# Optimization experiments

Hardware: AMD Instinct MI355X
Metric: run time of the kernel (lower is better)

The kernel has to match this reference:

```python
import jax, jax.numpy as jnp
import numpy as np

NEG_SLOPE = 0.2  # PyG GATConv default negative_slope


def _gat_layer(x, src, dst, W, a_src, a_dst, b, num_nodes):
    # x: [N, Fin] -> h: [N, Fout]
    h = x @ W
    # per-node attention logits (heads=1)
    alpha_s = h @ a_src  # [N]
    alpha_d = h @ a_dst  # [N]
    # edge scores e_ij = LeakyReLU(a_src . h_j + a_dst . h_i), j=src, i=dst
    e = alpha_s[src] + alpha_d[dst]
    e = jnp.where(e >= 0, e, NEG_SLOPE * e)
    # segment softmax over edges sharing the same destination node
    e_max = jax.ops.segment_max(e, dst, num_segments=num_nodes)  # [N]
    w = jnp.exp(e - e_max[dst])  # [E]
    denom = jax.ops.segment_sum(w, dst, num_segments=num_nodes)  # [N]
    alpha = w / denom[dst]  # [E]
    # weighted scatter-sum of source messages into destinations
    out = jax.ops.segment_sum(h[src] * alpha[:, None], dst, num_segments=num_nodes)
    return out + b


def _add_self_loops(edge_index, num_nodes):
    loops = jnp.arange(num_nodes, dtype=edge_index.dtype)
    src = jnp.concatenate([edge_index[0], loops])
    dst = jnp.concatenate([edge_index[1], loops])
    return src, dst


def setup_inputs() -> dict:
    key = jax.random.key(0)
    ks = jax.random.split(key, 8)
    N, E, F_in, F_hid, F_out = 50000, 800000, 128, 128, 64
    inp = {
        "node_features": jax.random.normal(ks[0], (N, F_in), dtype=jnp.float32),
        "edge_index": jax.random.randint(ks[1], (2, E), 0, N, dtype=jnp.int32),
        "W1": jax.random.normal(ks[2], (F_in, F_hid), dtype=jnp.float32) / np.sqrt(F_in),
        "a_src1": jax.random.normal(ks[3], (F_hid,), dtype=jnp.float32) / np.sqrt(F_hid),
        "a_dst1": jax.random.normal(ks[4], (F_hid,), dtype=jnp.float32) / np.sqrt(F_hid),
        "b1": jnp.zeros((F_hid,), dtype=jnp.float32),
        "W2": jax.random.normal(ks[5], (F_hid, F_out), dtype=jnp.float32) / np.sqrt(F_hid),
        "a_src2": jax.random.normal(ks[6], (F_out,), dtype=jnp.float32) / np.sqrt(F_out),
        "a_dst2": jax.random.normal(ks[7], (F_out,), dtype=jnp.float32) / np.sqrt(F_out),
        "b2": jnp.zeros((F_out,), dtype=jnp.float32),
    }
    return inp


def reference(node_features, edge_index, W1, a_src1, a_dst1, b1, W2, a_src2, a_dst2, b2):
    num_nodes = node_features.shape[0]
    src, dst = _add_self_loops(edge_index, num_nodes)
    x = _gat_layer(node_features, src, dst, W1, a_src1, a_dst1, b1, num_nodes)
    x = jax.nn.relu(x)
    x = _gat_layer(x, src, dst, W2, a_src2, a_dst2, b2, num_nodes)
    return x
```

## Files before the change

kernel.cpp:

```cpp
#include <hip/hip_runtime.h>
#include <hip/hip_fp16.h>
#include <cstddef>

#define NEG_SLOPE 0.2f
#define TILE 4096
#define CSR_CAP 6144

typedef _Float16 h8 __attribute__((ext_vector_type(8)));
typedef _Float16 h4 __attribute__((ext_vector_type(4)));
typedef float f4 __attribute__((ext_vector_type(4)));

__device__ __forceinline__ float leaky(float x) { return x >= 0.f ? x : NEG_SLOPE * x; }

__device__ __forceinline__ int wave_iscan(int v, int lane) {
#pragma unroll
    for (int off = 1; off < 64; off <<= 1) {
        int t = __shfl_up(v, off);
        if (lane >= off) v += t;
    }
    return v;
}

__global__ __launch_bounds__(256) void prep(
    const float* __restrict__ W1, const float* __restrict__ W2,
    _Float16* __restrict__ W1t, _Float16* __restrict__ W2t,
    int* __restrict__ bfill)
{
    const int b = blockIdx.x;
    const int tid = threadIdx.x;
    if (b == 0) bfill[tid] = 0;
    if (b < 8) {
        for (int i = b * 2048 + tid; i < (b + 1) * 2048; i += 256) {
            int n = i >> 7, k = i & 127;
            W1t[n * 128 + k] = (_Float16)W1[k * 128 + n];
        }
    } else {
        const int bb = b - 8;
        for (int i = bb * 2048 + tid; i < (bb + 1) * 2048; i += 256) {
            int n = i >> 7, k = i & 127;
            W2t[n * 128 + k] = (_Float16)W2[k * 64 + n];
        }
    }
}

__global__ __launch_bounds__(256) void gemm1_scatter(
    const float* __restrict__ x, const _Float16* __restrict__ Wg,
    const float* __restrict__ a_s, const float* __restrict__ a_d,
    _Float16* __restrict__ hh, float* __restrict__ alphaS, float* __restrict__ alphaD,
    int N, int nblk_gemm,
    const int* __restrict__ src, const int* __restrict__ dst,
    int* __restrict__ bfill, unsigned* __restrict__ staging, int cap, int E)
{
    constexpr int K = 128;
    constexpr int LDK = K + 8;
    constexpr int F = 128;
    constexpr int NT = F / 16;

    __shared__ union {
        struct { _Float16 As[64 * LDK]; _Float16 Wt[F * LDK]; } g;
        struct {
            int lcnt[256]; int loff[256]; int gbase[256]; int ws[4];
            unsigned pairs[TILE]; unsigned char bkt[TILE];
        } s;
    } u;

    const int tid = threadIdx.x;

    if (blockIdx.x < (unsigned)nblk_gemm) {
        const int wave = tid >> 6;
        const int lane = tid & 63;
        const int q = lane >> 4;
        const int c = lane & 15;
        const int rowb = blockIdx.x * 64;

        for (int i = tid; i < 64 * (K / 4); i += 256) {
            int r = i >> 5, c4 = i & 31;
            int gr = rowb + r;
            float4 v = (gr < N) ? *(const float4*)(x + (size_t)gr * K + c4 * 4)
                                : make_float4(0.f, 0.f, 0.f, 0.f);
            h4 hv = { (_Float16)v.x, (_Float16)v.y, (_Float16)v.z, (_Float16)v.w };
            *(h4*)(u.g.As + r * LDK + c4 * 4) = hv;
        }
        for (int i = tid; i < F * (K / 8); i += 256) {
            int n = i >> 4, k8 = i & 15;
            *(h8*)(u.g.Wt + n * LDK + k8 * 8) = *(const h8*)(Wg + n * 128 + k8 * 8);
        }
        __syncthreads();

        f4 acc[NT];
#pragma unroll
        for (int nt = 0; nt < NT; nt++) acc[nt] = (f4)0.f;

        const _Float16* aw = u.g.As + (wave * 16 + c) * LDK + q * 8;
#pragma unroll
        for (int kt = 0; kt < 4; kt++) {
            h8 af = *(const h8*)(aw + kt * 32);
#pragma unroll
            for (int nt = 0; nt < NT; nt++) {
                h8 bf = *(const h8*)(u.g.Wt + (nt * 16 + c) * LDK + kt * 32 + q * 8);
                acc[nt] = __builtin_amdgcn_mfma_f32_16x16x32_f16(af, bf, acc[nt], 0, 0, 0);
            }
        }

        float asl[NT], adl[NT];
#pragma unroll
        for (int nt = 0; nt < NT; nt++) {
            asl[nt] = a_s[nt * 16 + c];
            adl[nt] = a_d[nt * 16 + c];
        }
        const int row0 = rowb + wave * 16 + q * 4;
#pragma unroll
        for (int r = 0; r < 4; r++) {
            int row = row0 + r;
            if (row < N) {
                float ps = 0.f, pd = 0.f;
#pragma unroll
                for (int nt = 0; nt < NT; nt++) {
                    float v = acc[nt][r];
                    hh[(size_t)row * F + nt * 16 + c] = (_Float16)v;
                    ps += v * asl[nt];
                    pd += v * adl[nt];
                }
#pragma unroll
                for (int off = 8; off >= 1; off >>= 1) {
                    ps += __shfl_down(ps, off, 16);
                    pd += __shfl_down(pd, off, 16);
                }
                if (c == 0) { alphaS[row] = ps; alphaD[row] = pd; }
            }
        }
    } else {
        const int base = (blockIdx.x - nblk_gemm) * TILE;
        const int vt = min(TILE, E - base);

        u.s.lcnt[tid] = 0;
        __syncthreads();

        int d[TILE / 256], s[TILE / 256], r[TILE / 256];
#pragma unroll
        for (int j = 0; j < TILE / 256; j++) {
            int idx = base + j * 256 + tid;
            if (idx < E) {
                d[j] = dst[idx]; s[j] = src[idx];
                r[j] = atomicAdd(&u.s.lcnt[d[j] >> 8], 1);
            } else d[j] = -1;
        }
        __syncthreads();
        {
            int lane = tid & 63, wid = tid >> 6;
            int v = u.s.lcnt[tid];
            int incl = wave_iscan(v, lane);
            if (lane == 63) u.s.ws[wid] = incl;
            __syncthreads();
            int woff = 0;
            for (int w = 0; w < wid; w++) woff += u.s.ws[w];
            u.s.loff[tid] = woff + incl - v;
        }
        __syncthreads();
        {
            int c = u.s.lcnt[tid];
            if (c > 0) u.s.gbase[tid] = tid * cap + atomicAdd(&bfill[tid], c);
        }
        __syncthreads();
#pragma unroll
        for (int j = 0; j < TILE / 256; j++) {
            if (d[j] >= 0) {
                int b = d[j] >> 8;
                int slot = u.s.loff[b] + r[j];
                u.s.pairs[slot] = ((unsigned)d[j] << 16) | (unsigned)s[j];
                u.s.bkt[slot] = (unsigned char)b;
            }
        }
        __syncthreads();
        for (int slot = tid; slot < vt; slot += 256) {
            int b = u.s.bkt[slot];
            staging[u.s.gbase[b] + (slot - u.s.loff[b])] = u.s.pairs[slot];
        }
    }
}

template <int F, typename IT>
__global__ __launch_bounds__(256) void gemm_mfma(
    const IT* __restrict__ x, const _Float16* __restrict__ Wg,
    const float* __restrict__ a_s, const float* __restrict__ a_d,
    _Float16* __restrict__ hh, float* __restrict__ alphaS, float* __restrict__ alphaD,
    int N)
{
    constexpr int K = 128;
    constexpr int LDK = K + 8;
    constexpr int NT = F / 16;

    __shared__ _Float16 As[64 * LDK];
    __shared__ _Float16 Wt[F * LDK];

    const int tid = threadIdx.x;
    const int wave = tid >> 6;
    const int lane = tid & 63;
    const int q = lane >> 4;
    const int c = lane & 15;
    const int rowb = blockIdx.x * 64;

    if constexpr (sizeof(IT) == 4) {
        for (int i = tid; i < 64 * (K / 4); i += 256) {
            int r = i >> 5, c4 = i & 31;
            int gr = rowb + r;
            float4 v = (gr < N) ? *(const float4*)((const float*)x + (size_t)gr * K + c4 * 4)
                                : make_float4(0.f, 0.f, 0.f, 0.f);
            h4 hv = { (_Float16)v.x, (_Float16)v.y, (_Float16)v.z, (_Float16)v.w };
            *(h4*)(As + r * LDK + c4 * 4) = hv;
        }
    } else {
        for (int i = tid; i < 64 * (K / 8); i += 256) {
            int r = i >> 4, c8 = i & 15;
            int gr = rowb + r;
            h8 v;
            if (gr < N) v = *(const h8*)((const _Float16*)x + (size_t)gr * K + c8 * 8);
            else        v = (h8)(_Float16)0.f;
            *(h8*)(As + r * LDK + c8 * 8) = v;
        }
    }
    for (int i = tid; i < F * (K / 8); i += 256) {
        int n = i >> 4, k8 = i & 15;
        *(h8*)(Wt + n * LDK + k8 * 8) = *(const h8*)(Wg + n * 128 + k8 * 8);
    }
    __syncthreads();

    f4 acc[NT];
#pragma unroll
    for (int nt = 0; nt < NT; nt++) acc[nt] = (f4)0.f;

    const _Float16* aw = As + (wave * 16 + c) * LDK + q * 8;
#pragma unroll
    for (int kt = 0; kt < 4; kt++) {
        h8 af = *(const h8*)(aw + kt * 32);
#pragma unroll
        for (int nt = 0; nt < NT; nt++) {
            h8 bf = *(const h8*)(Wt + (nt * 16 + c) * LDK + kt * 32 + q * 8);
            acc[nt] = __builtin_amdgcn_mfma_f32_16x16x32_f16(af, bf, acc[nt], 0, 0, 0);
        }
    }

    float asl[NT], adl[NT];
#pragma unroll
    for (int nt = 0; nt < NT; nt++) {
        asl[nt] = a_s[nt * 16 + c];
        adl[nt] = a_d[nt * 16 + c];
    }
    const int row0 = rowb + wave * 16 + q * 4;
#pragma unroll
    for (int r = 0; r < 4; r++) {
        int row = row0 + r;
        if (row < N) {
            float ps = 0.f, pd = 0.f;
#pragma unroll
            for (int nt = 0; nt < NT; nt++) {
                float v = acc[nt][r];
                hh[(size_t)row * F + nt * 16 + c] = (_Float16)v;
                ps += v * asl[nt];
                pd += v * adl[nt];
            }
#pragma unroll
            for (int off = 8; off >= 1; off >>= 1) {
                ps += __shfl_down(ps, off, 16);
                pd += __shfl_down(pd, off, 16);
            }
            if (c == 0) { alphaS[row] = ps; alphaD[row] = pd; }
        }
    }
}

__global__ __launch_bounds__(512) void bucket_to_csr(
    const unsigned* __restrict__ staging, const int* __restrict__ bfill,
    int* __restrict__ row_start, int* __restrict__ row_end,
    int* __restrict__ src_sorted, int cap, int N)
{
    __shared__ unsigned lp[CSR_CAP];
    __shared__ int lcnt[256], loff[256], lfill[256];
    __shared__ int ws[4];
    const int tid = threadIdx.x;
    const int b = blockIdx.x;
    const int beg = b * cap;
    const int len = bfill[b];

    if (tid < 256) lcnt[tid] = 0;
    __syncthreads();
    for (int p = tid; p < len; p += 512) {
        unsigned u = staging[beg + p];
        lp[p] = u;
        atomicAdd(&lcnt[(u >> 16) & 255], 1);
    }
    __syncthreads();
    {
        int lane = tid & 63, wid = tid >> 6;
        int v = 0, incl = 0;
        if (tid < 256) {
            v = lcnt[tid];
            incl = wave_iscan(v, lane);
            if (lane == 63) ws[wid] = incl;
        }
        __syncthreads();
        if (tid < 256) {
            int woff = 0;
            for (int w = 0; w < wid; w++) woff += ws[w];
            int excl = woff + incl - v;
            loff[tid] = excl;
            lfill[tid] = excl;
            int node = (b << 8) + tid;
            if (node < N) { row_start[node] = beg + excl; row_end[node] = beg + excl + v; }
        }
    }
    __syncthreads();
    for (int p = tid; p < len; p += 512) {
        unsigned u = lp[p];
        int pos = atomicAdd(&lfill[(u >> 16) & 255], 1);
        src_sorted[beg + pos] = (int)(u & 0xFFFFu);
    }
}

template <int F, bool RELU, typename OT>
__global__ __launch_bounds__(256) void gat_aggregate(
    const int* __restrict__ row_start, const int* __restrict__ row_end,
    const int* __restrict__ src_sorted, const __half* __restrict__ hh,
    const float* __restrict__ aS, const float* __restrict__ aD,
    const float* __restrict__ bias, OT* __restrict__ out, int N)
{
    constexpr int LPE = F / 8;
    constexpr int EPW = 64 / LPE;

    const int i = blockIdx.x * 4 + (threadIdx.x >> 6);
    if (i >= N) return;
    const int lane = threadIdx.x & 63;
    const int sub = lane / LPE;
    const int l = lane % LPE;

    const float adi = aD[i];
    const int start = row_start[i];
    const int end = row_end[i];

    float accA[8], accB[8];
#pragma unroll
    for (int q = 0; q < 8; q++) { accA[q] = 0.f; accB[q] = 0.f; }
    float denA = 0.f, denB = 0.f;

    int e = start + sub;
    int s0 = (e + 0 * EPW < end) ? src_sorted[e + 0 * EPW] : -1;
    int s1 = (e + 1 * EPW < end) ? src_sorted[e + 1 * EPW] : -1;
    int s2 = (e + 2 * EPW < end) ? src_sorted[e + 2 * EPW] : -1;
    int s3 = (e + 3 * EPW < end) ? src_sorted[e + 3 * EPW] : -1;

    while (s0 >= 0) {
        int eb = e + 4 * EPW;
        int n0 = (eb + 0 * EPW < end) ? src_sorted[eb + 0 * EPW] : -1;
        int n1 = (eb + 1 * EPW < end) ? src_sorted[eb + 1 * EPW] : -1;
        int n2 = (eb + 2 * EPW < end) ? src_sorted[eb + 2 * EPW] : -1;
        int n3 = (eb + 3 * EPW < end) ? src_sorted[eb + 3 * EPW] : -1;

        {
            float w = __expf(leaky(aS[s0] + adi));
            uint4 u = *(const uint4*)(hh + (size_t)s0 * F + l * 8);
            const __half2* hp = (const __half2*)&u;
#pragma unroll
            for (int q = 0; q < 4; q++) {
                float2 f = __half22float2(hp[q]);
                accA[q * 2] += w * f.x; accA[q * 2 + 1] += w * f.y;
            }
            denA += w;
        }
        if (s1 >= 0) {
            float w = __expf(leaky(aS[s1] + adi));
            uint4 u = *(const uint4*)(hh + (size_t)s1 * F + l * 8);
            const __half2* hp = (const __half2*)&u;
#pragma unroll
            for (int q = 0; q < 4; q++) {
                float2 f = __half22float2(hp[q]);
                accB[q * 2] += w * f.x; accB[q * 2 + 1] += w * f.y;
            }
            denB += w;
        }
        if (s2 >= 0) {
            float w = __expf(leaky(aS[s2] + adi));
            uint4 u = *(const uint4*)(hh + (size_t)s2 * F + l * 8);
            const __half2* hp = (const __half2*)&u;
#pragma unroll
            for (int q = 0; q < 4; q++) {
                float2 f = __half22float2(hp[q]);
                accA[q * 2] += w * f.x; accA[q * 2 + 1] += w * f.y;
            }
            denA += w;
        }
        if (s3 >= 0) {
            float w = __expf(leaky(aS[s3] + adi));
            uint4 u = *(const uint4*)(hh + (size_t)s3 * F + l * 8);
            const __half2* hp = (const __half2*)&u;
#pragma unroll
            for (int q = 0; q < 4; q++) {
                float2 f = __half22float2(hp[q]);
                accB[q * 2] += w * f.x; accB[q * 2 + 1] += w * f.y;
            }
            denB += w;
        }
        e = eb;
        s0 = n0; s1 = n1; s2 = n2; s3 = n3;
    }

    float acc[8];
#pragma unroll
    for (int q = 0; q < 8; q++) acc[q] = accA[q] + accB[q];
    float denom = denA + denB;

#pragma unroll
    for (int off = 32; off >= LPE; off >>= 1) {
#pragma unroll
        for (int q = 0; q < 8; q++) acc[q] += __shfl_down(acc[q], off);
        denom += __shfl_down(denom, off);
    }

    if (sub == 0) {
        float wsf = __expf(leaky(aS[i] + adi));
        uint4 u = *(const uint4*)(hh + (size_t)i * F + l * 8);
        const __half2* hp = (const __half2*)&u;
        float inv = 1.f / (denom + wsf);
        float4 b0 = *(const float4*)(bias + l * 8);
        float4 b1 = *(const float4*)(bias + l * 8 + 4);
        float o[8];
#pragma unroll
        for (int q = 0; q < 4; q++) {
            float2 f = __half22float2(hp[q]);
            o[q * 2]     = (acc[q * 2]     + wsf * f.x) * inv;
            o[q * 2 + 1] = (acc[q * 2 + 1] + wsf * f.y) * inv;
        }
        o[0] += b0.x; o[1] += b0.y; o[2] += b0.z; o[3] += b0.w;
        o[4] += b1.x; o[5] += b1.y; o[6] += b1.z; o[7] += b1.w;
        if (RELU) {
#pragma unroll
            for (int q = 0; q < 8; q++) o[q] = fmaxf(o[q], 0.f);
        }
        if constexpr (sizeof(OT) == 2) {
            __half2 qh[4];
            qh[0] = __floats2half2_rn(o[0], o[1]);
            qh[1] = __floats2half2_rn(o[2], o[3]);
            qh[2] = __floats2half2_rn(o[4], o[5]);
            qh[3] = __floats2half2_rn(o[6], o[7]);
            *(uint4*)((__half*)out + (size_t)i * F + l * 8) = *(uint4*)qh;
        } else {
            *(float4*)((float*)out + (size_t)i * F + l * 8)     = make_float4(o[0], o[1], o[2], o[3]);
            *(float4*)((float*)out + (size_t)i * F + l * 8 + 4) = make_float4(o[4], o[5], o[6], o[7]);
        }
    }
}

extern "C" void kernel_launch(void* const* d_in, const int* in_sizes, int n_in,
                              void* d_out, int out_size, void* d_ws, size_t ws_size,
                              hipStream_t stream)
{
    const float* x   = (const float*)d_in[0];
    const int*   ei  = (const int*)d_in[1];
    const float* W1  = (const float*)d_in[2];
    const float* aS1 = (const float*)d_in[3];
    const float* aD1 = (const float*)d_in[4];
    const float* b1  = (const float*)d_in[5];
    const float* W2  = (const float*)d_in[6];
    const float* aS2 = (const float*)d_in[7];
    const float* aD2 = (const float*)d_in[8];
    const float* b2  = (const float*)d_in[9];

    const int K = 128, F1 = 128, F2 = 64;
    const int N = in_sizes[0] / K;
    const int E = in_sizes[1] / 2;
    const int* src = ei;
    const int* dst = ei + E;

    const int Np = (N + 4) & ~3;
    const int NB = (N + 255) >> 8;
    const int nbt = (E + TILE - 1) / TILE;
    const int nblk_gemm = (N + 63) / 64;
    int cap = (((E / NB) * 3) / 2 + 255) & ~255;
    if (cap > CSR_CAP) cap = CSR_CAP;

    char* wsb = (char*)d_ws;
    int* bfill        = (int*)wsb;      wsb += 256 * 4;
    _Float16* W1t     = (_Float16*)wsb; wsb += 128 * 128 * 2;
    _Float16* W2t     = (_Float16*)wsb; wsb += 64 * 128 * 2;
    int* row_start    = (int*)wsb;      wsb += (size_t)Np * 4;
    int* row_end      = (int*)wsb;      wsb += (size_t)Np * 4;
    unsigned* staging = (unsigned*)wsb; wsb += (size_t)NB * CSR_CAP * 4;
    int* src_sorted   = (int*)wsb;      wsb += (size_t)NB * CSR_CAP * 4;
    _Float16* hh1     = (_Float16*)wsb; wsb += (size_t)N * F1 * 2;
    _Float16* x2h     = (_Float16*)wsb; wsb += (size_t)N * F1 * 2;
    _Float16* hh2     = (_Float16*)wsb; wsb += (size_t)N * F2 * 2;
    float* as_        = (float*)wsb;    wsb += (size_t)Np * 4;
    float* ad_        = (float*)wsb;    wsb += (size_t)Np * 4;

    dim3 blk(256);

    prep<<<dim3(12), blk, 0, stream>>>(W1, W2, W1t, W2t, bfill);

    gemm1_scatter<<<dim3(nblk_gemm + nbt), blk, 0, stream>>>(
        x, W1t, aS1, aD1, hh1, as_, ad_, N, nblk_gemm,
        src, dst, bfill, staging, cap, E);

    bucket_to_csr<<<dim3(NB), dim3(512), 0, stream>>>(staging, bfill, row_start, row_end,
                                                      src_sorted, cap, N);

    gat_aggregate<F1, true, __half><<<dim3((N + 3) / 4), blk, 0, stream>>>(
        row_start, row_end, src_sorted, (const __half*)hh1, as_, ad_, b1,
        (__half*)x2h, N);

    gemm_mfma<F2, _Float16><<<dim3((N + 63) / 64), blk, 0, stream>>>(
        x2h, W2t, aS2, aD2, hh2, as_, ad_, N);

    gat_aggregate<F2, false, float><<<dim3((N + 3) / 4), blk, 0, stream>>>(
        row_start, row_end, src_sorted, (const __half*)hh2, as_, ad_, b2,
        (float*)d_out, N);
}
```

Measured before the change: 190.9 us.

## Fuse layer-1 aggregation with layer-2 GEMM and widen CSR build blocks

Measured after the change: 202.0 us. 5.8% more time.

```diff
diff --git a/kernel.cpp b/kernel.cpp
--- a/kernel.cpp
+++ b/kernel.cpp
@@ -179,97 +179,7 @@
     }
 }
 
-template <int F, typename IT>
-__global__ __launch_bounds__(256) void gemm_mfma(
-    const IT* __restrict__ x, const _Float16* __restrict__ Wg,
-    const float* __restrict__ a_s, const float* __restrict__ a_d,
-    _Float16* __restrict__ hh, float* __restrict__ alphaS, float* __restrict__ alphaD,
-    int N)
-{
-    constexpr int K = 128;
-    constexpr int LDK = K + 8;
-    constexpr int NT = F / 16;
-
-    __shared__ _Float16 As[64 * LDK];
-    __shared__ _Float16 Wt[F * LDK];
-
-    const int tid = threadIdx.x;
-    const int wave = tid >> 6;
-    const int lane = tid & 63;
-    const int q = lane >> 4;
-    const int c = lane & 15;
-    const int rowb = blockIdx.x * 64;
-
-    if constexpr (sizeof(IT) == 4) {
-        for (int i = tid; i < 64 * (K / 4); i += 256) {
-            int r = i >> 5, c4 = i & 31;
-            int gr = rowb + r;
-            float4 v = (gr < N) ? *(const float4*)((const float*)x + (size_t)gr * K + c4 * 4)
-                                : make_float4(0.f, 0.f, 0.f, 0.f);
-            h4 hv = { (_Float16)v.x, (_Float16)v.y, (_Float16)v.z, (_Float16)v.w };
-            *(h4*)(As + r * LDK + c4 * 4) = hv;
-        }
-    } else {
-        for (int i = tid; i < 64 * (K / 8); i += 256) {
-            int r = i >> 4, c8 = i & 15;
-            int gr = rowb + r;
-            h8 v;
-            if (gr < N) v = *(const h8*)((const _Float16*)x + (size_t)gr * K + c8 * 8);
-            else        v = (h8)(_Float16)0.f;
-            *(h8*)(As + r * LDK + c8 * 8) = v;
-        }
-    }
-    for (int i = tid; i < F * (K / 8); i += 256) {
-        int n = i >> 4, k8 = i & 15;
-        *(h8*)(Wt + n * LDK + k8 * 8) = *(const h8*)(Wg + n * 128 + k8 * 8);
-    }
-    __syncthreads();
-
-    f4 acc[NT];
-#pragma unroll
-    for (int nt = 0; nt < NT; nt++) acc[nt] = (f4)0.f;
-
-    const _Float16* aw = As + (wave * 16 + c) * LDK + q * 8;
-#pragma unroll
-    for (int kt = 0; kt < 4; kt++) {
-        h8 af = *(const h8*)(aw + kt * 32);
-#pragma unroll
-        for (int nt = 0; nt < NT; nt++) {
-            h8 bf = *(const h8*)(Wt + (nt * 16 + c) * LDK + kt * 32 + q * 8);
-            acc[nt] = __builtin_amdgcn_mfma_f32_16x16x32_f16(af, bf, acc[nt], 0, 0, 0);
-        }
-    }
-
-    float asl[NT], adl[NT];
-#pragma unroll
-    for (int nt = 0; nt < NT; nt++) {
-        asl[nt] = a_s[nt * 16 + c];
-        adl[nt] = a_d[nt * 16 + c];
-    }
-    const int row0 = rowb + wave * 16 + q * 4;
-#pragma unroll
-    for (int r = 0; r < 4; r++) {
-        int row = row0 + r;
-        if (row < N) {
-            float ps = 0.f, pd = 0.f;
-#pragma unroll
-            for (int nt = 0; nt < NT; nt++) {
-                float v = acc[nt][r];
-                hh[(size_t)row * F + nt * 16 + c] = (_Float16)v;
-                ps += v * asl[nt];
-                pd += v * adl[nt];
-            }
-#pragma unroll
-            for (int off = 8; off >= 1; off >>= 1) {
-                ps += __shfl_down(ps, off, 16);
-                pd += __shfl_down(pd, off, 16);
-            }
-            if (c == 0) { alphaS[row] = ps; alphaD[row] = pd; }
-        }
-    }
-}
-
-__global__ __launch_bounds__(512) void bucket_to_csr(
+__global__ __launch_bounds__(1024) void bucket_to_csr(
     const unsigned* __restrict__ staging, const int* __restrict__ bfill,
     int* __restrict__ row_start, int* __restrict__ row_end,
     int* __restrict__ src_sorted, int cap, int N)
@@ -284,7 +194,7 @@
 
     if (tid < 256) lcnt[tid] = 0;
     __syncthreads();
-    for (int p = tid; p < len; p += 512) {
+    for (int p = tid; p < len; p += 1024) {
         unsigned u = staging[beg + p];
         lp[p] = u;
         atomicAdd(&lcnt[(u >> 16) & 255], 1);
@@ -310,10 +220,199 @@
         }
     }
     __syncthreads();
-    for (int p = tid; p < len; p += 512) {
+    for (int p = tid; p < len; p += 1024) {
         unsigned u = lp[p];
         int pos = atomicAdd(&lfill[(u >> 16) & 255], 1);
         src_sorted[beg + pos] = (int)(u & 0xFFFFu);
+    }
+}
+
+__global__ __launch_bounds__(256) void agg1_gemm2(
+    const int* __restrict__ row_start, const int* __restrict__ row_end,
+    const int* __restrict__ src_sorted, const __half* __restrict__ hh1,
+    const float* __restrict__ aS1, const float* __restrict__ aD1,
+    const float* __restrict__ b1,
+    const _Float16* __restrict__ W2t,
+    const float* __restrict__ aS2, const float* __restrict__ aD2,
+    _Float16* __restrict__ hh2, float* __restrict__ alphaS2, float* __restrict__ alphaD2,
+    int N)
+{
+    constexpr int K = 128;
+    constexpr int LDK = K + 8;
+    constexpr int F2 = 64;
+    constexpr int NT = F2 / 16;
+
+    __shared__ _Float16 As[64 * LDK];
+    __shared__ _Float16 Wt[F2 * LDK];
+
+    const int tid = threadIdx.x;
+    const int wave = tid >> 6;
+    const int lane = tid & 63;
+    const int rowb = blockIdx.x * 64;
+
+    for (int i = tid; i < F2 * (K / 8); i += 256) {
+        int n = i >> 4, k8 = i & 15;
+        *(h8*)(Wt + n * LDK + k8 * 8) = *(const h8*)(W2t + n * 128 + k8 * 8);
+    }
+
+    const int sub = lane >> 4;
+    const int l = lane & 15;
+
+    for (int it = 0; it < 16; it++) {
+        const int r = wave * 16 + it;
+        const int i = rowb + r;
+        if (i < N) {
+            const float adi = aD1[i];
+            const int start = row_start[i];
+            const int end = row_end[i];
+
+            float accA[8], accB[8];
+#pragma unroll
+            for (int q = 0; q < 8; q++) { accA[q] = 0.f; accB[q] = 0.f; }
+            float denA = 0.f, denB = 0.f;
+
+            int e = start + sub;
+            int s0 = (e + 0 * 4 < end) ? src_sorted[e + 0 * 4] : -1;
+            int s1 = (e + 1 * 4 < end) ? src_sorted[e + 1 * 4] : -1;
+            int s2 = (e + 2 * 4 < end) ? src_sorted[e + 2 * 4] : -1;
+            int s3 = (e + 3 * 4 < end) ? src_sorted[e + 3 * 4] : -1;
+
+            while (s0 >= 0) {
+                int eb = e + 16;
+                int n0 = (eb + 0 * 4 < end) ? src_sorted[eb + 0 * 4] : -1;
+                int n1 = (eb + 1 * 4 < end) ? src_sorted[eb + 1 * 4] : -1;
+                int n2 = (eb + 2 * 4 < end) ? src_sorted[eb + 2 * 4] : -1;
+                int n3 = (eb + 3 * 4 < end) ? src_sorted[eb + 3 * 4] : -1;
+
+                {
+                    float w = __expf(leaky(aS1[s0] + adi));
+                    uint4 u = *(const uint4*)(hh1 + (size_t)s0 * 128 + l * 8);
+                    const __half2* hp = (const __half2*)&u;
+#pragma unroll
+                    for (int q = 0; q < 4; q++) {
+                        float2 f = __half22float2(hp[q]);
+                        accA[q * 2] += w * f.x; accA[q * 2 + 1] += w * f.y;
+                    }
+                    denA += w;
+                }
+                if (s1 >= 0) {
+                    float w = __expf(leaky(aS1[s1] + adi));
+                    uint4 u = *(const uint4*)(hh1 + (size_t)s1 * 128 + l * 8);
+                    const __half2* hp = (const __half2*)&u;
+#pragma unroll
+                    for (int q = 0; q < 4; q++) {
+                        float2 f = __half22float2(hp[q]);
+                        accB[q * 2] += w * f.x; accB[q * 2 + 1] += w * f.y;
+                    }
+                    denB += w;
+                }
+                if (s2 >= 0) {
+                    float w = __expf(leaky(aS1[s2] + adi));
+                    uint4 u = *(const uint4*)(hh1 + (size_t)s2 * 128 + l * 8);
+                    const __half2* hp = (const __half2*)&u;
+#pragma unroll
+                    for (int q = 0; q < 4; q++) {
+                        float2 f = __half22float2(hp[q]);
+                        accA[q * 2] += w * f.x; accA[q * 2 + 1] += w * f.y;
+                    }
+                    denA += w;
+                }
+                if (s3 >= 0) {
+                    float w = __expf(leaky(aS1[s3] + adi));
+                    uint4 u = *(const uint4*)(hh1 + (size_t)s3 * 128 + l * 8);
+                    const __half2* hp = (const __half2*)&u;
+#pragma unroll
+                    for (int q = 0; q < 4; q++) {
+                        float2 f = __half22float2(hp[q]);
+                        accB[q * 2] += w * f.x; accB[q * 2 + 1] += w * f.y;
+                    }
+                    denB += w;
+                }
+                e = eb;
+                s0 = n0; s1 = n1; s2 = n2; s3 = n3;
+            }
+
+            float acc[8];
+#pragma unroll
+            for (int q = 0; q < 8; q++) acc[q] = accA[q] + accB[q];
+            float denom = denA + denB;
+
+#pragma unroll
+            for (int off = 32; off >= 16; off >>= 1) {
+#pragma unroll
+                for (int q = 0; q < 8; q++) acc[q] += __shfl_down(acc[q], off);
+                denom += __shfl_down(denom, off);
+            }
+
+            if (sub == 0) {
+                float wsf = __expf(leaky(aS1[i] + adi));
+                uint4 u = *(const uint4*)(hh1 + (size_t)i * 128 + l * 8);
+                const __half2* hp = (const __half2*)&u;
+                float inv = 1.f / (denom + wsf);
+                float4 b0 = *(const float4*)(b1 + l * 8);
+                float4 bb1 = *(const float4*)(b1 + l * 8 + 4);
+                float o[8];
+#pragma unroll
+                for (int q = 0; q < 4; q++) {
+                    float2 f = __half22float2(hp[q]);
+                    o[q * 2]     = (acc[q * 2]     + wsf * f.x) * inv;
+                    o[q * 2 + 1] = (acc[q * 2 + 1] + wsf * f.y) * inv;
+                }
+                o[0] += b0.x; o[1] += b0.y; o[2] += b0.z; o[3] += b0.w;
+                o[4] += bb1.x; o[5] += bb1.y; o[6] += bb1.z; o[7] += bb1.w;
+                h8 hv;
+#pragma unroll
+                for (int q = 0; q < 8; q++) hv[q] = (_Float16)fmaxf(o[q], 0.f);
+                *(h8*)(As + r * LDK + l * 8) = hv;
+            }
+        }
+    }
+    __syncthreads();
+
+    const int q = lane >> 4;
+    const int c = lane & 15;
+
+    f4 acc[NT];
+#pragma unroll
+    for (int nt = 0; nt < NT; nt++) acc[nt] = (f4)0.f;
+
+    const _Float16* aw = As + (wave * 16 + c) * LDK + q * 8;
+#pragma unroll
+    for (int kt = 0; kt < 4; kt++) {
+        h8 af = *(const h8*)(aw + kt * 32);
+#pragma unroll
+        for (int nt = 0; nt < NT; nt++) {
+            h8 bf = *(const h8*)(Wt + (nt * 16 + c) * LDK + kt * 32 + q * 8);
+            acc[nt] = __builtin_amdgcn_mfma_f32_16x16x32_f16(af, bf, acc[nt], 0, 0, 0);
+        }
+    }
+
+    float asl[NT], adl[NT];
+#pragma unroll
+    for (int nt = 0; nt < NT; nt++) {
+        asl[nt] = aS2[nt * 16 + c];
+        adl[nt] = aD2[nt * 16 + c];
+    }
+    const int row0 = rowb + wave * 16 + q * 4;
+#pragma unroll
+    for (int r = 0; r < 4; r++) {
+        int row = row0 + r;
+        if (row < N) {
+            float ps = 0.f, pd = 0.f;
+#pragma unroll
+            for (int nt = 0; nt < NT; nt++) {
+                float v = acc[nt][r];
+                hh2[(size_t)row * F2 + nt * 16 + c] = (_Float16)v;
+                ps += v * asl[nt];
+                pd += v * adl[nt];
+            }
+#pragma unroll
+            for (int off = 8; off >= 1; off >>= 1) {
+                ps += __shfl_down(ps, off, 16);
+                pd += __shfl_down(pd, off, 16);
+            }
+            if (c == 0) { alphaS2[row] = ps; alphaD2[row] = pd; }
+        }
     }
 }
 
@@ -486,10 +585,11 @@
     unsigned* staging = (unsigned*)wsb; wsb += (size_t)NB * CSR_CAP * 4;
     int* src_sorted   = (int*)wsb;      wsb += (size_t)NB * CSR_CAP * 4;
     _Float16* hh1     = (_Float16*)wsb; wsb += (size_t)N * F1 * 2;
-    _Float16* x2h     = (_Float16*)wsb; wsb += (size_t)N * F1 * 2;
     _Float16* hh2     = (_Float16*)wsb; wsb += (size_t)N * F2 * 2;
     float* as_        = (float*)wsb;    wsb += (size_t)Np * 4;
     float* ad_        = (float*)wsb;    wsb += (size_t)Np * 4;
+    float* as2_       = (float*)wsb;    wsb += (size_t)Np * 4;
+    float* ad2_       = (float*)wsb;    wsb += (size_t)Np * 4;
 
     dim3 blk(256);
 
@@ -499,17 +599,14 @@
         x, W1t, aS1, aD1, hh1, as_, ad_, N, nblk_gemm,
         src, dst, bfill, staging, cap, E);
 
-    bucket_to_csr<<<dim3(NB), dim3(512), 0, stream>>>(staging, bfill, row_start, row_end,
-                                                      src_sorted, cap, N);
-
-    gat_aggregate<F1, true, __half><<<dim3((N + 3) / 4), blk, 0, stream>>>(
+    bucket_to_csr<<<dim3(NB), dim3(1024), 0, stream>>>(staging, bfill, row_start, row_end,
+                                                       src_sorted, cap, N);
+
+    agg1_gemm2<<<dim3(nblk_gemm), blk, 0, stream>>>(
         row_start, row_end, src_sorted, (const __half*)hh1, as_, ad_, b1,
-        (__half*)x2h, N);
-
-    gemm_mfma<F2, _Float16><<<dim3((N + 63) / 64), blk, 0, stream>>>(
-        x2h, W2t, aS2, aD2, hh2, as_, ad_, N);
+        W2t, aS2, aD2, hh2, as2_, ad2_, N);
 
     gat_aggregate<F2, false, float><<<dim3((N + 3) / 4), blk, 0, stream>>>(
-        row_start, row_end, src_sorted, (const __half*)hh2, as_, ad_, b2,
+        row_start, row_end, src_sorted, (const __half*)hh2, as2_, ad2_, b2,
         (float*)d_out, N);
 }
```

## Split layer-1 GEMM across scatter and CSR kernels to balance load

Applied to the files above, without the earlier changes.

Measured after the change: 189.2 us. Within noise of the previous version (-0.9%).

```diff
diff --git a/kernel.cpp b/kernel.cpp
--- a/kernel.cpp
+++ b/kernel.cpp
@@ -43,21 +43,93 @@
     }
 }
 
-__global__ __launch_bounds__(256) void gemm1_scatter(
+struct GemmLds { _Float16 As[64 * 136]; _Float16 Wt[128 * 136]; };
+
+__device__ __forceinline__ void gemm1_tile(
+    GemmLds& g, int tid, int rowb,
     const float* __restrict__ x, const _Float16* __restrict__ Wg,
     const float* __restrict__ a_s, const float* __restrict__ a_d,
     _Float16* __restrict__ hh, float* __restrict__ alphaS, float* __restrict__ alphaD,
-    int N, int nblk_gemm,
-    const int* __restrict__ src, const int* __restrict__ dst,
-    int* __restrict__ bfill, unsigned* __restrict__ staging, int cap, int E)
+    int N)
 {
     constexpr int K = 128;
     constexpr int LDK = K + 8;
     constexpr int F = 128;
     constexpr int NT = F / 16;
 
+    const int wave = tid >> 6;
+    const int lane = tid & 63;
+    const int q = lane >> 4;
+    const int c = lane & 15;
+
+    for (int i = tid; i < 64 * (K / 4); i += 256) {
+        int r = i >> 5, c4 = i & 31;
+        int gr = rowb + r;
+        float4 v = (gr < N) ? *(const float4*)(x + (size_t)gr * K + c4 * 4)
+                            : make_float4(0.f, 0.f, 0.f, 0.f);
+        h4 hv = { (_Float16)v.x, (_Float16)v.y, (_Float16)v.z, (_Float16)v.w };
+        *(h4*)(g.As + r * LDK + c4 * 4) = hv;
+    }
+    for (int i = tid; i < F * (K / 8); i += 256) {
+        int n = i >> 4, k8 = i & 15;
+        *(h8*)(g.Wt + n * LDK + k8 * 8) = *(const h8*)(Wg + n * 128 + k8 * 8);
+    }
+    __syncthreads();
+
+    f4 acc[NT];
+#pragma unroll
+    for (int nt = 0; nt < NT; nt++) acc[nt] = (f4)0.f;
+
+    const _Float16* aw = g.As + (wave * 16 + c) * LDK + q * 8;
+#pragma unroll
+    for (int kt = 0; kt < 4; kt++) {
+        h8 af = *(const h8*)(aw + kt * 32);
+#pragma unroll
+        for (int nt = 0; nt < NT; nt++) {
+            h8 bf = *(const h8*)(g.Wt + (nt * 16 + c) * LDK + kt * 32 + q * 8);
+            acc[nt] = __builtin_amdgcn_mfma_f32_16x16x32_f16(af, bf, acc[nt], 0, 0, 0);
+        }
+    }
+
+    float asl[NT], adl[NT];
+#pragma unroll
+    for (int nt = 0; nt < NT; nt++) {
+        asl[nt] = a_s[nt * 16 + c];
+        adl[nt] = a_d[nt * 16 + c];
+    }
+    const int row0 = rowb + wave * 16 + q * 4;
+#pragma unroll
+    for (int r = 0; r < 4; r++) {
+        int row = row0 + r;
+        if (row < N) {
+            float ps = 0.f, pd = 0.f;
+#pragma unroll
+            for (int nt = 0; nt < NT; nt++) {
+                float v = acc[nt][r];
+                hh[(size_t)row * F + nt * 16 + c] = (_Float16)v;
+                ps += v * asl[nt];
+                pd += v * adl[nt];
+            }
+#pragma unroll
+            for (int off = 8; off >= 1; off >>= 1) {
+                ps += __shfl_down(ps, off, 16);
+                pd += __shfl_down(pd, off, 16);
+            }
+            if (c == 0) { alphaS[row] = ps; alphaD[row] = pd; }
+        }
+    }
+}
+
+__global__ __launch_bounds__(256) void fatA(
+    const float* __restrict__ x, const _Float16* __restrict__ Wg,
+    const float* __restrict__ a_s, const float* __restrict__ a_d,
+    _Float16* __restrict__ hh, float* __restrict__ alphaS, float* __restrict__ alphaD,
+    int N, int gsplit,
+    const int* __restrict__ src, const int* __restrict__ dst,
+    int* __restrict__ bfill, unsigned* __restrict__ staging, int cap, int E)
+{
     __shared__ union {
-        struct { _Float16 As[64 * LDK]; _Float16 Wt[F * LDK]; } g;
+        GemmLds g;
         struct {
             int lcnt[256]; int loff[256]; int gbase[256]; int ws[4];
             unsigned pairs[TILE]; unsigned char bkt[TILE];
@@ -66,71 +138,10 @@
 
     const int tid = threadIdx.x;
 
-    if (blockIdx.x < (unsigned)nblk_gemm) {
-        const int wave = tid >> 6;
-        const int lane = tid & 63;
-        const int q = lane >> 4;
-        const int c = lane & 15;
-        const int rowb = blockIdx.x * 64;
-
-        for (int i = tid; i < 64 * (K / 4); i += 256) {
-            int r = i >> 5, c4 = i & 31;
-            int gr = rowb + r;
-            float4 v = (gr < N) ? *(const float4*)(x + (size_t)gr * K + c4 * 4)
-                                : make_float4(0.f, 0.f, 0.f, 0.f);
-            h4 hv = { (_Float16)v.x, (_Float16)v.y, (_Float16)v.z, (_Float16)v.w };
-            *(h4*)(u.g.As + r * LDK + c4 * 4) = hv;
-        }
-        for (int i = tid; i < F * (K / 8); i += 256) {
-            int n = i >> 4, k8 = i & 15;
-            *(h8*)(u.g.Wt + n * LDK + k8 * 8) = *(const h8*)(Wg + n * 128 + k8 * 8);
-        }
-        __syncthreads();
-
-        f4 acc[NT];
-#pragma unroll
-        for (int nt = 0; nt < NT; nt++) acc[nt] = (f4)0.f;
-
-        const _Float16* aw = u.g.As + (wave * 16 + c) * LDK + q * 8;
-#pragma unroll
-        for (int kt = 0; kt < 4; kt++) {
-            h8 af = *(const h8*)(aw + kt * 32);
-#pragma unroll
-            for (int nt = 0; nt < NT; nt++) {
-                h8 bf = *(const h8*)(u.g.Wt + (nt * 16 + c) * LDK + kt * 32 + q * 8);
-                acc[nt] = __builtin_amdgcn_mfma_f32_16x16x32_f16(af, bf, acc[nt], 0, 0, 0);
-            }
-        }
-
-        float asl[NT], adl[NT];
-#pragma unroll
-        for (int nt = 0; nt < NT; nt++) {
-            asl[nt] = a_s[nt * 16 + c];
-            adl[nt] = a_d[nt * 16 + c];
-        }
-        const int row0 = rowb + wave * 16 + q * 4;
-#pragma unroll
-        for (int r = 0; r < 4; r++) {
-            int row = row0 + r;
-            if (row < N) {
-                float ps = 0.f, pd = 0.f;
-#pragma unroll
-                for (int nt = 0; nt < NT; nt++) {
-                    float v = acc[nt][r];
-                    hh[(size_t)row * F + nt * 16 + c] = (_Float16)v;
-                    ps += v * asl[nt];
-                    pd += v * adl[nt];
-                }
-#pragma unroll
-                for (int off = 8; off >= 1; off >>= 1) {
-                    ps += __shfl_down(ps, off, 16);
-                    pd += __shfl_down(pd, off, 16);
-                }
-                if (c == 0) { alphaS[row] = ps; alphaD[row] = pd; }
-            }
-        }
+    if (blockIdx.x < (unsigned)gsplit) {
+        gemm1_tile(u.g, tid, blockIdx.x * 64, x, Wg, a_s, a_d, hh, alphaS, alphaD, N);
     } else {
-        const int base = (blockIdx.x - nblk_gemm) * TILE;
+        const int base = (blockIdx.x - gsplit) * TILE;
         const int vt = min(TILE, E - base);
 
         u.s.lcnt[tid] = 0;
@@ -179,6 +190,64 @@
     }
 }
 
+__global__ __launch_bounds__(256) void fatB(
+    const float* __restrict__ x, const _Float16* __restrict__ Wg,
+    const float* __restrict__ a_s, const float* __restrict__ a_d,
+    _Float16* __restrict__ hh, float* __restrict__ alphaS, float* __restrict__ alphaD,
+    int N, int gsplit, int ncsr,
+    const unsigned* __restrict__ staging, const int* __restrict__ bfill,
+    int* __restrict__ row_start, int* __restrict__ row_end,
+    int* __restrict__ src_sorted, int cap)
+{
+    __shared__ union {
+        GemmLds g;
+        struct {
+            unsigned lp[CSR_CAP];
+            int lcnt[256]; int loff[256]; int lfill[256]; int ws[4];
+        } c;
+    } u;
+
+    const int tid = threadIdx.x;
+
+    if (blockIdx.x >= (unsigned)ncsr) {
+        gemm1_tile(u.g, tid, (gsplit + blockIdx.x - ncsr) * 64,
+                   x, Wg, a_s, a_d, hh, alphaS, alphaD, N);
+    } else {
+        const int b = blockIdx.x;
+        const int beg = b * cap;
+        const int len = bfill[b];
+
+        u.c.lcnt[tid] = 0;
+        __syncthreads();
+        for (int p = tid; p < len; p += 256) {
+            unsigned v = staging[beg + p];
+            u.c.lp[p] = v;
+            atomicAdd(&u.c.lcnt[(v >> 16) & 255], 1);
+        }
+        __syncthreads();
+        {
+            int lane = tid & 63, wid = tid >> 6;
+            int v = u.c.lcnt[tid];
+            int incl = wave_iscan(v, lane);
+            if (lane == 63) u.c.ws[wid] = incl;
+            __syncthreads();
+            int woff = 0;
+            for (int w = 0; w < wid; w++) woff += u.c.ws[w];
+            int excl = woff + incl - v;
+            u.c.loff[tid] = excl;
+            u.c.lfill[tid] = excl;
+            int node = (b << 8) + tid;
+            if (node < N) { row_start[node] = beg + excl; row_end[node] = beg + excl + v; }
+        }
+        __syncthreads();
+        for (int p = tid; p < len; p += 256) {
+            unsigned v = u.c.lp[p];
+            int pos = atomicAdd(&u.c.lfill[(v >> 16) & 255], 1);
+            src_sorted[beg + pos] = (int)(v & 0xFFFFu);
+        }
+    }
+}
+
 template <int F, typename IT>
 __global__ __launch_bounds__(256) void gemm_mfma(
     const IT* __restrict__ x, const _Float16* __restrict__ Wg,
@@ -266,54 +335,6 @@
             }
             if (c == 0) { alphaS[row] = ps; alphaD[row] = pd; }
         }
-    }
-}
-
-__global__ __launch_bounds__(512) void bucket_to_csr(
-    const unsigned* __restrict__ staging, const int* __restrict__ bfill,
-    int* __restrict__ row_start, int* __restrict__ row_end,
-    int* __restrict__ src_sorted, int cap, int N)
-{
-    __shared__ unsigned lp[CSR_CAP];
-    __shared__ int lcnt[256], loff[256], lfill[256];
-    __shared__ int ws[4];
-    const int tid = threadIdx.x;
-    const int b = blockIdx.x;
-    const int beg = b * cap;
-    const int len = bfill[b];
-
-    if (tid < 256) lcnt[tid] = 0;
-    __syncthreads();
-    for (int p = tid; p < len; p += 512) {
-        unsigned u = staging[beg + p];
-        lp[p] = u;
-        atomicAdd(&lcnt[(u >> 16) & 255], 1);
-    }
-    __syncthreads();
-    {
-        int lane = tid & 63, wid = tid >> 6;
-        int v = 0, incl = 0;
-        if (tid < 256) {
-            v = lcnt[tid];
-            incl = wave_iscan(v, lane);
-            if (lane == 63) ws[wid] = incl;
-        }
-        __syncthreads();
-        if (tid < 256) {
-            int woff = 0;
-            for (int w = 0; w < wid; w++) woff += ws[w];
-            int excl = woff + incl - v;
-            loff[tid] = excl;
-            lfill[tid] = excl;
-            int node = (b << 8) + tid;
-            if (node < N) { row_start[node] = beg + excl; row_end[node] = beg + excl + v; }
-        }
-    }
-    __syncthreads();
-    for (int p = tid; p < len; p += 512) {
-        unsigned u = lp[p];
-        int pos = atomicAdd(&lfill[(u >> 16) & 255], 1);
-        src_sorted[beg + pos] = (int)(u & 0xFFFFu);
     }
 }
 
@@ -474,6 +495,7 @@
     const int NB = (N + 255) >> 8;
     const int nbt = (E + TILE - 1) / TILE;
     const int nblk_gemm = (N + 63) / 64;
+    const int gsplit = (nblk_gemm * 5) / 8;
     int cap = (((E / NB) * 3) / 2 + 255) & ~255;
     if (cap > CSR_CAP) cap = CSR_CAP;
 
@@ -490,26 +512,29 @@
     _Float16* hh2     = (_Float16*)wsb; wsb += (size_t)N * F2 * 2;
     float* as_        = (float*)wsb;    wsb += (size_t)Np * 4;
     float* ad_        = (float*)wsb;    wsb += (size_t)Np * 4;
+    float* as2_       = (float*)wsb;    wsb += (size_t)Np * 4;
+    float* ad2_       = (float*)wsb;    wsb += (size_t)Np * 4;
 
     dim3 blk(256);
 
     prep<<<dim3(12), blk, 0, stream>>>(W1, W2, W1t, W2t, bfill);
 
-    gemm1_scatter<<<dim3(nblk_gemm + nbt), blk, 0, stream>>>(
-        x, W1t, aS1, aD1, hh1, as_, ad_, N, nblk_gemm,
+    fatA<<<dim3(gsplit + nbt), blk, 0, stream>>>(
+        x, W1t, aS1, aD1, hh1, as_, ad_, N, gsplit,
         src, dst, bfill, staging, cap, E);
 
-    bucket_to_csr<<<dim3(NB), dim3(512), 0, stream>>>(staging, bfill, row_start, row_end,
-                                                      src_sorted, cap, N);
+    fatB<<<dim3(NB + (nblk_gemm - gsplit)), blk, 0, stream>>>(
+        x, W1t, aS1, aD1, hh1, as_, ad_, N, gsplit, NB,
+        staging, bfill, row_start, row_end, src_sorted, cap);
 
     gat_aggregate<F1, true, __half><<<dim3((N + 3) / 4), blk, 0, stream>>>(
         row_start, row_end, src_sorted, (const __half*)hh1, as_, ad_, b1,
         (__half*)x2h, N);
 
     gemm_mfma<F2, _Float16><<<dim3((N + 63) / 64), blk, 0, stream>>>(
-        x2h, W2t, aS2, aD2, hh2, as_, ad_, N);
+        x2h, W2t, aS2, aD2, hh2, as2_, ad2_, N);
 
     gat_aggregate<F2, false, float><<<dim3((N + 3) / 4), blk, 0, stream>>>(
-        row_start, row_end, src_sorted, (const __half*)hh2, as_, ad_, b2,
+        row_start, row_end, src_sorted, (const __half*)hh2, as2_, ad2_, b2,
         (float*)d_out, N);
 }
```
